# Kernel tuning notes

Hardware: AMD Instinct MI355X
Metric: run time of the kernel (lower is better)

## Reference

```python
import jax, jax.numpy as jnp
import numpy as np

IN_F, OUT_F, RANK = 4096, 4096, 8
TOKENS = 8192


def setup_inputs() -> dict:
    key = jax.random.key(0)
    k1, k2, k3 = jax.random.split(key, 3)
    x = jax.random.normal(k1, (TOKENS, IN_F), dtype=jnp.float32)
    # xavier-uniform-ish init scale for the TT cores
    lim0 = float(np.sqrt(6.0 / (OUT_F + RANK)))
    lim1 = float(np.sqrt(6.0 / (RANK + IN_F)))
    core0 = jax.random.uniform(k2, (1, OUT_F, RANK), minval=-lim0, maxval=lim0, dtype=jnp.float32)
    core1 = jax.random.uniform(k3, (RANK, IN_F, 1), minval=-lim1, maxval=lim1, dtype=jnp.float32)
    bias = jnp.zeros((OUT_F,), dtype=jnp.float32)
    return {"x": x, "core0": core0, "core1": core1, "bias": bias}


def reference(x, core0, core1, bias):
    # Faithful to torch: weight[o, i] = sum_r core0[0, o, r] * core1[r, i, 0]
    # (original einsum 'ior, ri1 -> oi' with the size-1 leading/trailing dims broadcast)
    weight = jnp.einsum('or,ri->oi', core0[0], core1[:, :, 0])  # [OUT_F, IN_F]
    # F.linear: x @ weight.T + bias
    return x @ weight.T + bias
```

## Files before the change

kernel.cpp:

```cpp
#include <hip/hip_runtime.h>


#define TOKENS 8192
#define IN_F   4096
#define OUT_F  4096
#define RANK   8

__global__ __launch_bounds__(256) void tt_fused(const float* __restrict__ x,
                                                const float* __restrict__ core0,
                                                const float* __restrict__ core1,
                                                const float* __restrict__ bias,
                                                float* __restrict__ out) {
    __shared__ float y_s[8][RANK];

    const int tid  = threadIdx.x;
    const int wave = tid >> 6;
    const int lane = tid & 63;
    const int t0   = blockIdx.x * 8;

    const float* x0 = x + (size_t)(t0 + wave * 2) * IN_F;
    const float* x1 = x0 + IN_F;

    float acc0[RANK], acc1[RANK];
    #pragma unroll
    for (int r = 0; r < RANK; ++r) { acc0[r] = 0.f; acc1[r] = 0.f; }

    #pragma unroll 4
    for (int k = 0; k < 16; ++k) {
        const int i = 4 * (lane + 64 * k);
        const float4 a0 = *(const float4*)(x0 + i);
        const float4 a1 = *(const float4*)(x1 + i);
        #pragma unroll
        for (int r = 0; r < RANK; ++r) {
            const float4 c = *(const float4*)(core1 + r * IN_F + i);
            acc0[r] += a0.x * c.x + a0.y * c.y + a0.z * c.z + a0.w * c.w;
            acc1[r] += a1.x * c.x + a1.y * c.y + a1.z * c.z + a1.w * c.w;
        }
    }

    #pragma unroll
    for (int r = 0; r < RANK; ++r) {
        #pragma unroll
        for (int off = 32; off > 0; off >>= 1) {
            acc0[r] += __shfl_xor(acc0[r], off, 64);
            acc1[r] += __shfl_xor(acc1[r], off, 64);
        }
    }

    if (lane == 0) {
        #pragma unroll
        for (int r = 0; r < RANK; ++r) {
            y_s[wave * 2][r]     = acc0[r];
            y_s[wave * 2 + 1][r] = acc1[r];
        }
    }
    __syncthreads();

    #pragma unroll
    for (int j = 0; j < 4; ++j) {
        const int o = j * 1024 + tid * 4;

        float4 w[8];
        #pragma unroll
        for (int q = 0; q < 4; ++q) {
            w[2 * q]     = *(const float4*)(core0 + (o + q) * RANK);
            w[2 * q + 1] = *(const float4*)(core0 + (o + q) * RANK + 4);
        }
        const float4 b = *(const float4*)(bias + o);

        #pragma unroll
        for (int t = 0; t < 8; ++t) {
            const float4 y0 = *(const float4*)(&y_s[t][0]);
            const float4 y1 = *(const float4*)(&y_s[t][4]);
            float4 c;
            c.x = b.x + y0.x * w[0].x + y0.y * w[0].y + y0.z * w[0].z + y0.w * w[0].w
                      + y1.x * w[1].x + y1.y * w[1].y + y1.z * w[1].z + y1.w * w[1].w;
            c.y = b.y + y0.x * w[2].x + y0.y * w[2].y + y0.z * w[2].z + y0.w * w[2].w
                      + y1.x * w[3].x + y1.y * w[3].y + y1.z * w[3].z + y1.w * w[3].w;
            c.z = b.z + y0.x * w[4].x + y0.y * w[4].y + y0.z * w[4].z + y0.w * w[4].w
                      + y1.x * w[5].x + y1.y * w[5].y + y1.z * w[5].z + y1.w * w[5].w;
            c.w = b.w + y0.x * w[6].x + y0.y * w[6].y + y0.z * w[6].z + y0.w * w[6].w
                      + y1.x * w[7].x + y1.y * w[7].y + y1.z * w[7].z + y1.w * w[7].w;
            *(float4*)(out + (size_t)(t0 + t) * OUT_F + o) = c;
        }
    }
}

extern "C" void kernel_launch(void* const* d_in, const int* in_sizes, int n_in,
                              void* d_out, int out_size, void* d_ws, size_t ws_size,
                              hipStream_t stream) {
    const float* x     = (const float*)d_in[0];
    const float* core0 = (const float*)d_in[1];
    const float* core1 = (const float*)d_in[2];
    const float* bias  = (const float*)d_in[3];
    float* out = (float*)d_out;

    tt_fused<<<TOKENS / 8, 256, 0, stream>>>(x, core0, core1, bias, out);
}
```

Baseline: 280.5 us.

## Stage core1 chunks in double-buffered LDS and prefetch x rows

The rank projection now streams core1 through a double-buffered shared-memory tile in 512-column chunks, so each block loads core1 once per chunk from global memory instead of having every wave reload it. Each token is handled by half a wave (32 threads), and the next chunk of x and core1 is prefetched into registers while the current chunk is computed. Occupancy is hinted with launch_bounds(256,4). The cost is 32 KB of LDS per block, one barrier per chunk, and more live registers, all of which can limit occupancy.

```diff
diff --git a/kernel.cpp b/kernel.cpp
--- a/kernel.cpp
+++ b/kernel.cpp
@@ -5,60 +5,97 @@
 #define IN_F   4096
 #define OUT_F  4096
 #define RANK   8
+#define TPB_T  8
+#define CHUNK  512
+#define NCHUNK (IN_F / CHUNK)
 
-__global__ __launch_bounds__(256) void tt_fused(const float* __restrict__ x,
-                                                const float* __restrict__ core0,
-                                                const float* __restrict__ core1,
-                                                const float* __restrict__ bias,
-                                                float* __restrict__ out) {
-    __shared__ float y_s[8][RANK];
+__global__ __launch_bounds__(256, 4) void tt_fused2(const float* __restrict__ x,
+                                                    const float* __restrict__ core0,
+                                                    const float* __restrict__ core1,
+                                                    const float* __restrict__ bias,
+                                                    float* __restrict__ out) {
+    __shared__ float c1s[2][RANK][CHUNK];
+    __shared__ float y_s[TPB_T][RANK];
 
-    const int tid  = threadIdx.x;
-    const int wave = tid >> 6;
-    const int lane = tid & 63;
-    const int t0   = blockIdx.x * 8;
+    const int tid   = threadIdx.x;
+    const int t0    = blockIdx.x * TPB_T;
+    const int t_loc = tid >> 5;
+    const int j     = tid & 31;
 
-    const float* x0 = x + (size_t)(t0 + wave * 2) * IN_F;
-    const float* x1 = x0 + IN_F;
+    const float* xrow = x + (size_t)(t0 + t_loc) * IN_F;
 
-    float acc0[RANK], acc1[RANK];
     #pragma unroll
-    for (int r = 0; r < RANK; ++r) { acc0[r] = 0.f; acc1[r] = 0.f; }
+    for (int m = 0; m < 4; ++m) {
+        const int idx = tid + 256 * m;
+        const int r = idx >> 7, c4 = idx & 127;
+        *(float4*)&c1s[0][r][c4 * 4] = *(const float4*)(core1 + r * IN_F + c4 * 4);
+    }
+    float4 xv[4];
+    #pragma unroll
+    for (int g = 0; g < 4; ++g)
+        xv[g] = *(const float4*)(xrow + j * 4 + g * 128);
+    __syncthreads();
 
-    #pragma unroll 4
-    for (int k = 0; k < 16; ++k) {
-        const int i = 4 * (lane + 64 * k);
-        const float4 a0 = *(const float4*)(x0 + i);
-        const float4 a1 = *(const float4*)(x1 + i);
+    float acc[RANK];
+    #pragma unroll
+    for (int r = 0; r < RANK; ++r) acc[r] = 0.f;
+
+    for (int c = 0; c < NCHUNK; ++c) {
+        const int buf = c & 1;
+
+        float4 xn[4];
+        if (c + 1 < NCHUNK) {
+            #pragma unroll
+            for (int g = 0; g < 4; ++g)
+                xn[g] = *(const float4*)(xrow + (c + 1) * CHUNK + j * 4 + g * 128);
+        }
+        float4 st[4];
+        if (c + 1 < NCHUNK) {
+            #pragma unroll
+            for (int m = 0; m < 4; ++m) {
+                const int idx = tid + 256 * m;
+                const int r = idx >> 7, c4 = idx & 127;
+                st[m] = *(const float4*)(core1 + r * IN_F + (c + 1) * CHUNK + c4 * 4);
+            }
+        }
+
         #pragma unroll
-        for (int r = 0; r < RANK; ++r) {
-            const float4 c = *(const float4*)(core1 + r * IN_F + i);
-            acc0[r] += a0.x * c.x + a0.y * c.y + a0.z * c.z + a0.w * c.w;
-            acc1[r] += a1.x * c.x + a1.y * c.y + a1.z * c.z + a1.w * c.w;
+        for (int g = 0; g < 4; ++g) {
+            #pragma unroll
+            for (int r = 0; r < RANK; ++r) {
+                const float4 cv = *(const float4*)&c1s[buf][r][j * 4 + g * 128];
+                acc[r] += xv[g].x * cv.x + xv[g].y * cv.y
+                        + xv[g].z * cv.z + xv[g].w * cv.w;
+            }
         }
+
+        if (c + 1 < NCHUNK) {
+            #pragma unroll
+            for (int m = 0; m < 4; ++m) {
+                const int idx = tid + 256 * m;
+                const int r = idx >> 7, c4 = idx & 127;
+                *(float4*)&c1s[buf ^ 1][r][c4 * 4] = st[m];
+            }
+            #pragma unroll
+            for (int g = 0; g < 4; ++g) xv[g] = xn[g];
+        }
+        __syncthreads();
     }
 
     #pragma unroll
     for (int r = 0; r < RANK; ++r) {
         #pragma unroll
-        for (int off = 32; off > 0; off >>= 1) {
-            acc0[r] += __shfl_xor(acc0[r], off, 64);
-            acc1[r] += __shfl_xor(acc1[r], off, 64);
-        }
+        for (int off = 1; off <= 16; off <<= 1)
+            acc[r] += __shfl_xor(acc[r], off, 64);
     }
-
-    if (lane == 0) {
+    if (j == 0) {
         #pragma unroll
-        for (int r = 0; r < RANK; ++r) {
-            y_s[wave * 2][r]     = acc0[r];
-            y_s[wave * 2 + 1][r] = acc1[r];
-        }
+        for (int r = 0; r < RANK; ++r) y_s[t_loc][r] = acc[r];
     }
     __syncthreads();
 
-    #pragma unroll
-    for (int j = 0; j < 4; ++j) {
-        const int o = j * 1024 + tid * 4;
+    for (int jj = 0; jj < 4; ++jj) {
+        const int o = jj * 1024 + tid * 4;
 
         float4 w[8];
         #pragma unroll
@@ -69,19 +106,19 @@
         const float4 b = *(const float4*)(bias + o);
 
         #pragma unroll
-        for (int t = 0; t < 8; ++t) {
+        for (int t = 0; t < TPB_T; ++t) {
             const float4 y0 = *(const float4*)(&y_s[t][0]);
             const float4 y1 = *(const float4*)(&y_s[t][4]);
-            float4 c;
-            c.x = b.x + y0.x * w[0].x + y0.y * w[0].y + y0.z * w[0].z + y0.w * w[0].w
-                      + y1.x * w[1].x + y1.y * w[1].y + y1.z * w[1].z + y1.w * w[1].w;
-            c.y = b.y + y0.x * w[2].x + y0.y * w[2].y + y0.z * w[2].z + y0.w * w[2].w
-                      + y1.x * w[3].x + y1.y * w[3].y + y1.z * w[3].z + y1.w * w[3].w;
-            c.z = b.z + y0.x * w[4].x + y0.y * w[4].y + y0.z * w[4].z + y0.w * w[4].w
-                      + y1.x * w[5].x + y1.y * w[5].y + y1.z * w[5].z + y1.w * w[5].w;
-            c.w = b.w + y0.x * w[6].x + y0.y * w[6].y + y0.z * w[6].z + y0.w * w[6].w
-                      + y1.x * w[7].x + y1.y * w[7].y + y1.z * w[7].z + y1.w * w[7].w;
-            *(float4*)(out + (size_t)(t0 + t) * OUT_F + o) = c;
+            float4 cc;
+            cc.x = b.x + y0.x * w[0].x + y0.y * w[0].y + y0.z * w[0].z + y0.w * w[0].w
+                       + y1.x * w[1].x + y1.y * w[1].y + y1.z * w[1].z + y1.w * w[1].w;
+            cc.y = b.y + y0.x * w[2].x + y0.y * w[2].y + y0.z * w[2].z + y0.w * w[2].w
+                       + y1.x * w[3].x + y1.y * w[3].y + y1.z * w[3].z + y1.w * w[3].w;
+            cc.z = b.z + y0.x * w[4].x + y0.y * w[4].y + y0.z * w[4].z + y0.w * w[4].w
+                       + y1.x * w[5].x + y1.y * w[5].y + y1.z * w[5].z + y1.w * w[5].w;
+            cc.w = b.w + y0.x * w[6].x + y0.y * w[6].y + y0.z * w[6].z + y0.w * w[6].w
+                       + y1.x * w[7].x + y1.y * w[7].y + y1.z * w[7].z + y1.w * w[7].w;
+            *(float4*)(out + (size_t)(t0 + t) * OUT_F + o) = cc;
         }
     }
 }
@@ -95,5 +132,5 @@
     const float* bias  = (const float*)d_in[3];
     float* out = (float*)d_out;
 
-    tt_fused<<<TOKENS / 8, 256, 0, stream>>>(x, core0, core1, bias, out);
+    tt_fused2<<<TOKENS / TPB_T, 256, 0, stream>>>(x, core0, core1, bias, out);
 }
```

New measurement: 297.7 us. 6.1% more time.
